# Performance work log

Hardware: AMD Instinct MI355X
Metric: run time of the kernel (lower is better)

Reference implementation:

```python
import jax, jax.numpy as jnp
from jax import lax
import numpy as np

U = 128  # num_units
F = 64   # input features
OUT = 6  # dense head units


def _lstm_layer(x, W, R, b):
    """Keras-style LSTM (gate order i,f,g,o; sigmoid recurrent act, tanh act).
    x: [B,T,D], W: [D,4U], R: [U,4U], b: [4U]. Returns (all_h [B,T,U], last_h [B,U])."""
    B = x.shape[0]
    xw = jnp.einsum('btd,dk->btk', x, W) + b  # precompute input projection [B,T,4U]

    def step(carry, xw_t):
        h, c = carry
        z = xw_t + h @ R  # [B,4U]
        i, f, g, o = jnp.split(z, 4, axis=-1)
        i = jax.nn.sigmoid(i)
        f = jax.nn.sigmoid(f)
        g = jnp.tanh(g)
        o = jax.nn.sigmoid(o)
        c = f * c + i * g
        h = o * jnp.tanh(c)
        return (h, c), h

    h0 = jnp.zeros((B, U), dtype=x.dtype)
    c0 = jnp.zeros((B, U), dtype=x.dtype)
    (h_last, _), hs = lax.scan(step, (h0, c0), jnp.swapaxes(xw, 0, 1))
    return jnp.swapaxes(hs, 0, 1), h_last


def setup_inputs() -> dict:
    key = jax.random.key(0)
    ks = jax.random.split(key, 12)
    s = 0.05
    inp = {
        'x': jax.random.normal(ks[0], (256, 512, F), dtype=jnp.float32),
        'W0': jax.random.normal(ks[1], (F, 4 * U), dtype=jnp.float32) * s,
        'R0': jax.random.normal(ks[2], (U, 4 * U), dtype=jnp.float32) * s,
        'b0': jnp.zeros((4 * U,), dtype=jnp.float32),
        'W1': jax.random.normal(ks[3], (U, 4 * U), dtype=jnp.float32) * s,
        'R1': jax.random.normal(ks[4], (U, 4 * U), dtype=jnp.float32) * s,
        'b1': jnp.zeros((4 * U,), dtype=jnp.float32),
        'W2': jax.random.normal(ks[5], (U, 4 * U), dtype=jnp.float32) * s,
        'R2': jax.random.normal(ks[6], (U, 4 * U), dtype=jnp.float32) * s,
        'b2': jnp.zeros((4 * U,), dtype=jnp.float32),
        'Wd': jax.random.normal(ks[7], (U, OUT), dtype=jnp.float32) * s,
        'bd': jnp.zeros((OUT,), dtype=jnp.float32),
    }
    return inp


def reference(x, W0, R0, b0, W1, R1, b1, W2, R2, b2, Wd, bd):
    h, _ = _lstm_layer(x, W0, R0, b0)      # [B,T,U]
    h, _ = _lstm_layer(h, W1, R1, b1)      # [B,T,U]
    _, h_last = _lstm_layer(h, W2, R2, b2) # [B,U] (return_sequences=False)
    return h_last @ Wd + bd                # [B,6]
```

## Files before the change

### kernel.cpp

```cpp
#include <hip/hip_runtime.h>
#include <cstdint>
#include <cstddef>

#define U4    512
#define UNITS 128
#define BATCH 256
#define TSEQ  512
#define FEAT  64
#define SEQS  8
#define NBLK  (BATCH / SEQS)

typedef short short8 __attribute__((ext_vector_type(8)));
typedef float f32x4  __attribute__((ext_vector_type(4)));

#define MFMA_BF16(C, A, B) \
    asm("v_mfma_f32_16x16x32_bf16 %0, %1, %2, %0" : "+v"(C) : "v"(A), "a"(B))

__device__ __forceinline__ void barrier_lds_only() {
    __builtin_amdgcn_sched_barrier(0);
    asm volatile("s_waitcnt lgkmcnt(0)" ::: "memory");
    __builtin_amdgcn_s_barrier();
    __builtin_amdgcn_sched_barrier(0);
}

__device__ __forceinline__ float sigm(float x) {
    float e = __expf(-x);
    return __fdividef(1.0f, 1.0f + e);
}
__device__ __forceinline__ float tanh_fast(float x) {
    float e = __expf(2.0f * x);
    return 1.0f - __fdividef(2.0f, e + 1.0f);
}

__device__ __forceinline__ unsigned short f2bf(float f) {
    unsigned u = __float_as_uint(f);
    unsigned r = u + 0x7FFFu + ((u >> 16) & 1u);
    return (unsigned short)(r >> 16);
}
__device__ __forceinline__ float bf2f(unsigned short h) {
    return __uint_as_float(((unsigned)h) << 16);
}

__global__ __launch_bounds__(256)
void rw_frag(const float* __restrict__ R0, const float* __restrict__ R1,
             const float* __restrict__ R2,
             const float* __restrict__ W0, const float* __restrict__ W1,
             const float* __restrict__ W2,
             unsigned short* __restrict__ Rf, unsigned short* __restrict__ Wf)
{
    if (blockIdx.x < 192) {
        int gid = blockIdx.x * 256 + threadIdx.x;
        int l    = gid >> 14;
        int r    = gid & 16383;
        int lane = r & 63;
        int fi   = r >> 6;
        int pass = fi & 1;
        int kt   = (fi >> 1) & 3;
        int gate = (fi >> 3) & 3;
        int w    = fi >> 5;
        const float* R = (l == 0) ? R0 : (l == 1) ? R1 : R2;

        int col = gate * UNITS + w * 16 + (lane & 15);
        int k0  = kt * 32 + (lane >> 4) * 8;
        short8 v;
        #pragma unroll
        for (int j = 0; j < 8; ++j) {
            float x = R[(size_t)(k0 + j) * U4 + col];
            unsigned short hi = f2bf(x);
            unsigned short s = pass ? f2bf(x - bf2f(hi)) : hi;
            v[j] = (short)s;
        }
        *(short8*)(Rf + (size_t)gid * 8) = v;
    } else {
        int gid = (blockIdx.x - 192) * 256 + threadIdx.x;
        int l    = gid >> 14;
        int r    = gid & 16383;
        int lane = r & 63;
        int fi   = r >> 6;
        int pass = fi & 1;
        int kt   = (fi >> 1) & 3;
        int nt   = fi >> 3;
        const float* W = (l == 0) ? W0 : (l == 1) ? W1 : W2;
        const int K = (l == 0) ? FEAT : UNITS;

        int col = nt * 16 + (lane & 15);
        int k0  = kt * 32 + (lane >> 4) * 8;
        short8 v;
        #pragma unroll
        for (int j = 0; j < 8; ++j) {
            float x = (k0 + j < K) ? W[(size_t)(k0 + j) * U4 + col] : 0.f;
            unsigned short hi = f2bf(x);
            unsigned short s = pass ? f2bf(x - bf2f(hi)) : hi;
            v[j] = (short)s;
        }
        *(short8*)(Wf + (size_t)gid * 8) = v;
    }
}

struct PCell {
    const float* in;
    float* out;
    const unsigned short* wf;
    const float* bias;
    int sB, sT, t0, K;
};
struct PStage { PCell c[3]; };

__global__ __launch_bounds__(512, 2)
void proj_mfma(PStage ps, int tcShift)
{
    const PCell ce = ps.c[blockIdx.y];
    const int tid  = threadIdx.x;
    const int lane = tid & 63;
    const int w    = tid >> 6;
    const int m    = lane & 15;
    const int quad = lane >> 4;
    const int TcMask = (1 << tcShift) - 1;
    const int m0 = blockIdx.x * 64;

    __shared__ __align__(16) unsigned short atab[8][16][136];

    short8 bf[4][4][2];
    #pragma unroll
    for (int nt = 0; nt < 4; ++nt)
        #pragma unroll
        for (int kt = 0; kt < 4; ++kt)
            #pragma unroll
            for (int pp = 0; pp < 2; ++pp)
                bf[nt][kt][pp] = *(const short8*)(
                    ce.wf + ((size_t)((((w * 4 + nt) * 4 + kt) * 2) + pp) * 64 + lane) * 8);

    const float* __restrict__ inp = ce.in;
    #pragma unroll
    for (int rep = 0; rep < 16; ++rep) {
        int idx = rep * 512 + tid;
        int row = idx >> 7;
        int k   = idx & 127;
        int rg  = m0 + row;
        int b = rg >> tcShift, tc = rg & TcMask;
        float x = 0.f;
        if (k < ce.K)
            x = inp[(size_t)b * ce.sB + (size_t)(ce.t0 + tc) * ce.sT + k];
        unsigned short hi = f2bf(x);
        atab[row >> 3][2 * (row & 7)][k]     = hi;
        atab[row >> 3][2 * (row & 7) + 1][k] = f2bf(x - bf2f(hi));
    }
    __syncthreads();

    float bb[4];
    #pragma unroll
    for (int nt = 0; nt < 4; ++nt) bb[nt] = ce.bias[w * 64 + nt * 16 + m];

    float* __restrict__ outp = ce.out;
    #pragma unroll 1
    for (int r = 0; r < 8; ++r) {
        short8 af[4];
        #pragma unroll
        for (int kt = 0; kt < 4; ++kt)
            af[kt] = *(const short8*)(&atab[r][m][kt * 32 + quad * 8]);

        f32x4 C[4];
        #pragma unroll
        for (int nt = 0; nt < 4; ++nt) C[nt] = f32x4{0.f, 0.f, 0.f, 0.f};

        #pragma unroll
        for (int kt = 0; kt < 4; ++kt)
            #pragma unroll
            for (int pp = 0; pp < 2; ++pp)
                #pragma unroll
                for (int nt = 0; nt < 4; ++nt)
                    MFMA_BF16(C[nt], af[kt], bf[nt][kt][pp]);

        int row0 = m0 + r * 8 + 2 * quad;
        #pragma unroll
        for (int nt = 0; nt < 4; ++nt) {
            float z0 = C[nt].x + C[nt].y + bb[nt];
            float z1 = C[nt].z + C[nt].w + bb[nt];
            int col = w * 64 + nt * 16 + m;
            outp[(size_t)row0 * U4 + col]       = z0;
            outp[(size_t)(row0 + 1) * U4 + col] = z1;
        }
    }
}

struct Cell {
    const float* xw;
    const unsigned short* rf;
    float* hs;
    float* cs;
    float* hout;
    int init;
    int pad_;
};
struct StageArgs { Cell c[3]; };

__global__ __launch_bounds__(512, 2)
void lstm_rec(StageArgs sa, int Tc)
{
    const Cell ce = sa.c[blockIdx.y];
    const float* __restrict__ xw = ce.xw;
    const unsigned short* __restrict__ Rf = ce.rf;
    float* __restrict__ h_state = ce.hs;
    float* __restrict__ c_state = ce.cs;
    float* __restrict__ h_out = ce.hout;
    const int init = ce.init;

    const int tid  = threadIdx.x;
    const int blk  = blockIdx.x;
    const int lane = tid & 63;
    const int w    = tid >> 6;
    const int m    = lane & 15;
    const int quad = lane >> 4;

    __shared__ __align__(16) unsigned short htab[2][16][136];

    short8 bf[4][4][2];
    #pragma unroll
    for (int g = 0; g < 4; ++g)
        #pragma unroll
        for (int kt = 0; kt < 4; ++kt)
            #pragma unroll
            for (int pp = 0; pp < 2; ++pp)
                bf[g][kt][pp] = *(const short8*)(
                    Rf + ((size_t)((((w * 4 + g) * 4 + kt) * 2) + pp) * 64 + lane) * 8);

    const int unit = w * 16 + m;
    const int s0   = 2 * quad;
    const int s1   = s0 + 1;

    float c0 = 0.f, c1 = 0.f;
    if (!init) {
        c0 = c_state[(blk * SEQS + s0) * UNITS + unit];
        c1 = c_state[(blk * SEQS + s1) * UNITS + unit];
    }
    {
        int uu = tid & 127;
        #pragma unroll
        for (int i = 0; i < 2; ++i) {
            int s = (tid >> 7) + i * 4;
            float hv = init ? 0.f : h_state[(blk * SEQS + s) * UNITS + uu];
            unsigned short hi = f2bf(hv);
            htab[0][2 * s][uu]     = hi;
            htab[0][2 * s + 1][uu] = f2bf(hv - bf2f(hi));
        }
    }
    __syncthreads();

    const float* xw0 = xw + (size_t)(blk * SEQS + s0) * Tc * U4 + unit;
    const float* xw1 = xw + (size_t)(blk * SEQS + s1) * Tc * U4 + unit;

    float xa[8], xb[8];
    #pragma unroll
    for (int g = 0; g < 4; ++g) {
        xa[g]     = xw0[g * UNITS];
        xa[4 + g] = xw1[g * UNITS];
    }
    {
        const size_t o1 = (size_t)((Tc > 1) ? 1 : 0) * U4;
        #pragma unroll
        for (int g = 0; g < 4; ++g) {
            xb[g]     = xw0[o1 + g * UNITS];
            xb[4 + g] = xw1[o1 + g * UNITS];
        }
    }

    float hl0 = 0.f, hl1 = 0.f;

    auto STEP = [&](int t, int p, float (&xc)[8]) {
        short8 af[4];
        #pragma unroll
        for (int kt = 0; kt < 4; ++kt)
            af[kt] = *(const short8*)(&htab[p][m][kt * 32 + quad * 8]);

        f32x4 C0 = {xc[0], 0.f, xc[4], 0.f};
        f32x4 C1 = {xc[1], 0.f, xc[5], 0.f};
        f32x4 C2 = {xc[2], 0.f, xc[6], 0.f};
        f32x4 C3 = {xc[3], 0.f, xc[7], 0.f};

        int tp = t + 2; if (tp >= Tc) tp = Tc - 1;
        const size_t off = (size_t)tp * U4;
        #pragma unroll
        for (int g = 0; g < 4; ++g) {
            xc[g]     = xw0[off + g * UNITS];
            xc[4 + g] = xw1[off + g * UNITS];
        }

        __builtin_amdgcn_s_setprio(1);
        #pragma unroll
        for (int kt = 0; kt < 4; ++kt) {
            #pragma unroll
            for (int pp = 0; pp < 2; ++pp) {
                MFMA_BF16(C0, af[kt], bf[0][kt][pp]);
                MFMA_BF16(C1, af[kt], bf[1][kt][pp]);
            }
        }

        float zi0 = C0.x + C0.y, zi1 = C0.z + C0.w;
        float zf0 = C1.x + C1.y, zf1 = C1.z + C1.w;
        float iv0 = sigm(zi0), iv1 = sigm(zi1);
        float fv0 = sigm(zf0), fv1 = sigm(zf1);

        #pragma unroll
        for (int kt = 0; kt < 4; ++kt) {
            #pragma unroll
            for (int pp = 0; pp < 2; ++pp) {
                MFMA_BF16(C2, af[kt], bf[2][kt][pp]);
                MFMA_BF16(C3, af[kt], bf[3][kt][pp]);
            }
        }
        __builtin_amdgcn_s_setprio(0);

        float zg0 = C2.x + C2.y, zg1 = C2.z + C2.w;
        float zo0 = C3.x + C3.y, zo1 = C3.z + C3.w;

        float gv0 = tanh_fast(zg0), ov0 = sigm(zo0);
        c0 = __builtin_fmaf(fv0, c0, iv0 * gv0);
        float hv0 = ov0 * tanh_fast(c0);

        float gv1 = tanh_fast(zg1), ov1 = sigm(zo1);
        c1 = __builtin_fmaf(fv1, c1, iv1 * gv1);
        float hv1 = ov1 * tanh_fast(c1);

        hl0 = hv0; hl1 = hv1;

        unsigned short hi0 = f2bf(hv0);
        htab[p ^ 1][4 * quad + 0][unit] = hi0;
        htab[p ^ 1][4 * quad + 1][unit] = f2bf(hv0 - bf2f(hi0));
        unsigned short hi1 = f2bf(hv1);
        htab[p ^ 1][4 * quad + 2][unit] = hi1;
        htab[p ^ 1][4 * quad + 3][unit] = f2bf(hv1 - bf2f(hi1));

        if (h_out) {
            h_out[((size_t)(blk * SEQS + s0) * Tc + t) * UNITS + unit] = hv0;
            h_out[((size_t)(blk * SEQS + s1) * Tc + t) * UNITS + unit] = hv1;
        }
        barrier_lds_only();
    };

    #pragma unroll 1
    for (int t = 0; t < Tc; t += 2) {
        STEP(t,     0, xa);
        STEP(t + 1, 1, xb);
    }

    c_state[(blk * SEQS + s0) * UNITS + unit] = c0;
    c_state[(blk * SEQS + s1) * UNITS + unit] = c1;
    h_state[(blk * SEQS + s0) * UNITS + unit] = hl0;
    h_state[(blk * SEQS + s1) * UNITS + unit] = hl1;
}

__global__ __launch_bounds__(256)
void dense_head(const float* __restrict__ h2, const float* __restrict__ Wd,
                const float* __restrict__ bd, float* __restrict__ out)
{
    int b = threadIdx.x;
    float acc[6];
    #pragma unroll
    for (int o = 0; o < 6; ++o) acc[o] = bd[o];
    #pragma unroll 4
    for (int k = 0; k < UNITS; ++k) {
        float hv = h2[b * UNITS + k];
        #pragma unroll
        for (int o = 0; o < 6; ++o)
            acc[o] = __builtin_fmaf(hv, Wd[k * 6 + o], acc[o]);
    }
    #pragma unroll
    for (int o = 0; o < 6; ++o) out[b * 6 + o] = acc[o];
}

extern "C" void kernel_launch(void* const* d_in, const int* in_sizes, int n_in,
                              void* d_out, int out_size, void* d_ws, size_t ws_size,
                              hipStream_t stream)
{
    (void)in_sizes; (void)n_in; (void)out_size;
    const float* x  = (const float*)d_in[0];
    const float* Ws[3] = {(const float*)d_in[1], (const float*)d_in[4], (const float*)d_in[7]};
    const float* Rs[3] = {(const float*)d_in[2], (const float*)d_in[5], (const float*)d_in[8]};
    const float* bs[3] = {(const float*)d_in[3], (const float*)d_in[6], (const float*)d_in[9]};
    const float* Wd = (const float*)d_in[10];
    const float* bd = (const float*)d_in[11];
    float* out = (float*)d_out;

    int tcShift = 6;
    while (tcShift > 2) {
        size_t need = ((size_t)1 << tcShift) * 1835008u + 2359296u;
        if (need <= ws_size) break;
        --tcShift;
    }
    const int Tc = 1 << tcShift;
    const int nCh = TSEQ / Tc;

    float* xw3 = (float*)d_ws;
    float* hc2 = xw3 + 3 * (size_t)BATCH * Tc * U4;
    float* hs  = hc2 + 2 * (size_t)BATCH * Tc * UNITS;
    float* cs  = hs + 3 * BATCH * UNITS;
    unsigned short* Rf = (unsigned short*)(cs + 3 * BATCH * UNITS);
    unsigned short* Wf = Rf + 3 * 131072;

    const size_t xwStride = (size_t)BATCH * Tc * U4;
    const size_t hcStride = (size_t)BATCH * Tc * UNITS;

    rw_frag<<<384, 256, 0, stream>>>(Rs[0], Rs[1], Rs[2], Ws[0], Ws[1], Ws[2], Rf, Wf);

    for (int s = 0; s <= nCh + 1; ++s) {
        int lo = s - (nCh - 1); if (lo < 0) lo = 0;
        int hi = (s < 2) ? s : 2;
        if (lo > hi) continue;

        PStage ps{};
        StageArgs sa{};
        int n = 0;
        for (int lam = lo; lam <= hi; ++lam) {
            int c = s - lam;
            ps.c[n].in   = (lam == 0) ? x : hc2 + (size_t)(lam - 1) * hcStride;
            ps.c[n].out  = xw3 + (size_t)lam * xwStride;
            ps.c[n].wf   = Wf + (size_t)lam * 131072;
            ps.c[n].bias = bs[lam];
            ps.c[n].sB   = (lam == 0) ? TSEQ * FEAT : Tc * UNITS;
            ps.c[n].sT   = (lam == 0) ? FEAT : UNITS;
            ps.c[n].t0   = (lam == 0) ? c * Tc : 0;
            ps.c[n].K    = (lam == 0) ? FEAT : UNITS;

            sa.c[n].xw   = xw3 + (size_t)lam * xwStride;
            sa.c[n].rf   = Rf + (size_t)lam * 131072;
            sa.c[n].hs   = hs + lam * BATCH * UNITS;
            sa.c[n].cs   = cs + lam * BATCH * UNITS;
            sa.c[n].hout = (lam < 2) ? (hc2 + (size_t)lam * hcStride) : nullptr;
            sa.c[n].init = (c == 0) ? 1 : 0;
            ++n;
        }
        proj_mfma<<<dim3(BATCH * Tc / 64, n), 512, 0, stream>>>(ps, tcShift);
        lstm_rec<<<dim3(NBLK, n), 512, 0, stream>>>(sa, Tc);
    }

    dense_head<<<1, 256, 0, stream>>>(hs + 2 * BATCH * UNITS, Wd, bd, out);
}
```

Before: 1.266 ms.

## Fuse next-chunk layer-0 projection into recurrent stage kernel and pack hidden-state splits

Layer-0 input projection for the next chunk now runs as extra blocks inside the same launch as the recurrent LSTM blocks. Its output goes to a double-buffered xw slot, so the projection work can fill CUs the 32-96 recurrent blocks leave idle. Hidden-state outputs for the next layer are stored as packed bf16 hi/lo pairs, so the following projection skips the float-to-bf16 split and reads 4-byte words. The cost is more workspace, a larger shared-memory footprint for recurrent blocks, and a separate projection launch for layers 1-2.

```diff
diff --git a/kernel.cpp b/kernel.cpp
--- a/kernel.cpp
+++ b/kernel.cpp
@@ -12,6 +12,7 @@
 
 typedef short short8 __attribute__((ext_vector_type(8)));
 typedef float f32x4  __attribute__((ext_vector_type(4)));
+typedef unsigned short tab_t[16][136];
 
 #define MFMA_BF16(C, A, B) \
     asm("v_mfma_f32_16x16x32_bf16 %0, %1, %2, %0" : "+v"(C) : "v"(A), "a"(B))
@@ -98,27 +99,24 @@
 }
 
 struct PCell {
-    const float* in;
+    const void* in;
     float* out;
     const unsigned short* wf;
     const float* bias;
-    int sB, sT, t0, K;
+    int sB, sT, t0, K, packed, pad_;
 };
-struct PStage { PCell c[3]; };
-
-__global__ __launch_bounds__(512, 2)
-void proj_mfma(PStage ps, int tcShift)
-{
-    const PCell ce = ps.c[blockIdx.y];
+struct PStage { PCell c[2]; };
+
+__device__ __forceinline__ void proj_body(const PCell& ce, int bx, int tcShift,
+                                          tab_t* __restrict__ atab)
+{
     const int tid  = threadIdx.x;
     const int lane = tid & 63;
     const int w    = tid >> 6;
     const int m    = lane & 15;
     const int quad = lane >> 4;
     const int TcMask = (1 << tcShift) - 1;
-    const int m0 = blockIdx.x * 64;
-
-    __shared__ __align__(16) unsigned short atab[8][16][136];
+    const int m0 = bx * 64;
 
     short8 bf[4][4][2];
     #pragma unroll
@@ -130,20 +128,35 @@
                 bf[nt][kt][pp] = *(const short8*)(
                     ce.wf + ((size_t)((((w * 4 + nt) * 4 + kt) * 2) + pp) * 64 + lane) * 8);
 
-    const float* __restrict__ inp = ce.in;
-    #pragma unroll
-    for (int rep = 0; rep < 16; ++rep) {
-        int idx = rep * 512 + tid;
-        int row = idx >> 7;
-        int k   = idx & 127;
-        int rg  = m0 + row;
-        int b = rg >> tcShift, tc = rg & TcMask;
-        float x = 0.f;
-        if (k < ce.K)
-            x = inp[(size_t)b * ce.sB + (size_t)(ce.t0 + tc) * ce.sT + k];
-        unsigned short hi = f2bf(x);
-        atab[row >> 3][2 * (row & 7)][k]     = hi;
-        atab[row >> 3][2 * (row & 7) + 1][k] = f2bf(x - bf2f(hi));
+    if (ce.packed) {
+        const unsigned int* __restrict__ inp = (const unsigned int*)ce.in;
+        #pragma unroll
+        for (int rep = 0; rep < 16; ++rep) {
+            int idx = rep * 512 + tid;
+            int row = idx >> 7;
+            int k   = idx & 127;
+            int rg  = m0 + row;
+            int b = rg >> tcShift, tc = rg & TcMask;
+            unsigned int u = inp[(size_t)b * ce.sB + (size_t)(ce.t0 + tc) * ce.sT + k];
+            atab[row >> 3][2 * (row & 7)][k]     = (unsigned short)(u & 0xFFFFu);
+            atab[row >> 3][2 * (row & 7) + 1][k] = (unsigned short)(u >> 16);
+        }
+    } else {
+        const float* __restrict__ inp = (const float*)ce.in;
+        #pragma unroll
+        for (int rep = 0; rep < 16; ++rep) {
+            int idx = rep * 512 + tid;
+            int row = idx >> 7;
+            int k   = idx & 127;
+            int rg  = m0 + row;
+            int b = rg >> tcShift, tc = rg & TcMask;
+            float x = 0.f;
+            if (k < ce.K)
+                x = inp[(size_t)b * ce.sB + (size_t)(ce.t0 + tc) * ce.sT + k];
+            unsigned short hi = f2bf(x);
+            atab[row >> 3][2 * (row & 7)][k]     = hi;
+            atab[row >> 3][2 * (row & 7) + 1][k] = f2bf(x - bf2f(hi));
+        }
     }
     __syncthreads();
 
@@ -183,36 +196,38 @@
     }
 }
 
+__global__ __launch_bounds__(512, 2)
+void proj_mfma(PStage ps, int tcShift)
+{
+    __shared__ __align__(16) unsigned short smem[8 * 16 * 136];
+    proj_body(ps.c[blockIdx.y], blockIdx.x, tcShift, (tab_t*)smem);
+}
+
 struct Cell {
     const float* xw;
     const unsigned short* rf;
     float* hs;
     float* cs;
-    float* hout;
+    unsigned int* hout;
     int init;
     int pad_;
 };
-struct StageArgs { Cell c[3]; };
-
-__global__ __launch_bounds__(512, 2)
-void lstm_rec(StageArgs sa, int Tc)
-{
-    const Cell ce = sa.c[blockIdx.y];
+
+__device__ __forceinline__ void lstm_body(const Cell& ce, int blk, int Tc,
+                                          tab_t* __restrict__ htab)
+{
     const float* __restrict__ xw = ce.xw;
     const unsigned short* __restrict__ Rf = ce.rf;
     float* __restrict__ h_state = ce.hs;
     float* __restrict__ c_state = ce.cs;
-    float* __restrict__ h_out = ce.hout;
+    unsigned int* __restrict__ h_out = ce.hout;
     const int init = ce.init;
 
     const int tid  = threadIdx.x;
-    const int blk  = blockIdx.x;
     const int lane = tid & 63;
     const int w    = tid >> 6;
     const int m    = lane & 15;
     const int quad = lane >> 4;
-
-    __shared__ __align__(16) unsigned short htab[2][16][136];
 
     short8 bf[4][4][2];
     #pragma unroll
@@ -294,7 +309,6 @@
                 MFMA_BF16(C1, af[kt], bf[1][kt][pp]);
             }
         }
-
         float zi0 = C0.x + C0.y, zi1 = C0.z + C0.w;
         float zf0 = C1.x + C1.y, zf1 = C1.z + C1.w;
         float iv0 = sigm(zi0), iv1 = sigm(zi1);
@@ -324,15 +338,19 @@
         hl0 = hv0; hl1 = hv1;
 
         unsigned short hi0 = f2bf(hv0);
+        unsigned short lo0 = f2bf(hv0 - bf2f(hi0));
         htab[p ^ 1][4 * quad + 0][unit] = hi0;
-        htab[p ^ 1][4 * quad + 1][unit] = f2bf(hv0 - bf2f(hi0));
+        htab[p ^ 1][4 * quad + 1][unit] = lo0;
         unsigned short hi1 = f2bf(hv1);
+        unsigned short lo1 = f2bf(hv1 - bf2f(hi1));
         htab[p ^ 1][4 * quad + 2][unit] = hi1;
-        htab[p ^ 1][4 * quad + 3][unit] = f2bf(hv1 - bf2f(hi1));
+        htab[p ^ 1][4 * quad + 3][unit] = lo1;
 
         if (h_out) {
-            h_out[((size_t)(blk * SEQS + s0) * Tc + t) * UNITS + unit] = hv0;
-            h_out[((size_t)(blk * SEQS + s1) * Tc + t) * UNITS + unit] = hv1;
+            h_out[((size_t)(blk * SEQS + s0) * Tc + t) * UNITS + unit] =
+                (unsigned int)hi0 | ((unsigned int)lo0 << 16);
+            h_out[((size_t)(blk * SEQS + s1) * Tc + t) * UNITS + unit] =
+                (unsigned int)hi1 | ((unsigned int)lo1 << 16);
         }
         barrier_lds_only();
     };
@@ -347,6 +365,24 @@
     c_state[(blk * SEQS + s1) * UNITS + unit] = c1;
     h_state[(blk * SEQS + s0) * UNITS + unit] = hl0;
     h_state[(blk * SEQS + s1) * UNITS + unit] = hl1;
+}
+
+struct FusedArgs {
+    Cell lc[3];
+    PCell pc;
+    int n_lstm;
+    int has_proj;
+};
+
+__global__ __launch_bounds__(512, 2)
+void stage_fused(FusedArgs fa, int Tc, int tcShift)
+{
+    __shared__ __align__(16) unsigned short smem[8 * 16 * 136];
+    int bx = blockIdx.x;
+    if (bx < fa.n_lstm * NBLK)
+        lstm_body(fa.lc[bx >> 5], bx & 31, Tc, (tab_t*)smem);
+    else
+        proj_body(fa.pc, bx - fa.n_lstm * NBLK, tcShift, (tab_t*)smem);
 }
 
 __global__ __launch_bounds__(256)
@@ -383,24 +419,33 @@
 
     int tcShift = 6;
     while (tcShift > 2) {
-        size_t need = ((size_t)1 << tcShift) * 1835008u + 2359296u;
+        size_t need = ((size_t)1 << tcShift) * 2359296u + 2359296u;
         if (need <= ws_size) break;
         --tcShift;
     }
     const int Tc = 1 << tcShift;
     const int nCh = TSEQ / Tc;
-
-    float* xw3 = (float*)d_ws;
-    float* hc2 = xw3 + 3 * (size_t)BATCH * Tc * U4;
-    float* hs  = hc2 + 2 * (size_t)BATCH * Tc * UNITS;
-    float* cs  = hs + 3 * BATCH * UNITS;
+    const int projGrid = BATCH * Tc / 64;
+
+    const size_t xwStride = (size_t)BATCH * Tc * U4;
+    const size_t hcStride = (size_t)BATCH * Tc * UNITS;
+
+    float* xw = (float*)d_ws;
+    unsigned int* hc = (unsigned int*)(xw + 4 * xwStride);
+    float* hs = (float*)(hc + 2 * hcStride);
+    float* cs = hs + 3 * BATCH * UNITS;
     unsigned short* Rf = (unsigned short*)(cs + 3 * BATCH * UNITS);
     unsigned short* Wf = Rf + 3 * 131072;
 
-    const size_t xwStride = (size_t)BATCH * Tc * U4;
-    const size_t hcStride = (size_t)BATCH * Tc * UNITS;
-
     rw_frag<<<384, 256, 0, stream>>>(Rs[0], Rs[1], Rs[2], Ws[0], Ws[1], Ws[2], Rf, Wf);
+
+    {
+        PStage ps{};
+        ps.c[0].in = x; ps.c[0].out = xw; ps.c[0].wf = Wf; ps.c[0].bias = bs[0];
+        ps.c[0].sB = TSEQ * FEAT; ps.c[0].sT = FEAT; ps.c[0].t0 = 0;
+        ps.c[0].K = FEAT; ps.c[0].packed = 0;
+        proj_mfma<<<dim3(projGrid, 1), 512, 0, stream>>>(ps, tcShift);
+    }
 
     for (int s = 0; s <= nCh + 1; ++s) {
         int lo = s - (nCh - 1); if (lo < 0) lo = 0;
@@ -408,29 +453,46 @@
         if (lo > hi) continue;
 
         PStage ps{};
-        StageArgs sa{};
+        int pn = 0;
+        int plo = (lo > 1) ? lo : 1;
+        for (int lam = plo; lam <= hi; ++lam) {
+            ps.c[pn].in   = hc + (size_t)(lam - 1) * hcStride;
+            ps.c[pn].out  = xw + (size_t)(1 + lam) * xwStride;
+            ps.c[pn].wf   = Wf + (size_t)lam * 131072;
+            ps.c[pn].bias = bs[lam];
+            ps.c[pn].sB   = Tc * UNITS;
+            ps.c[pn].sT   = UNITS;
+            ps.c[pn].t0   = 0;
+            ps.c[pn].K    = UNITS;
+            ps.c[pn].packed = 1;
+            ++pn;
+        }
+        if (pn) proj_mfma<<<dim3(projGrid, pn), 512, 0, stream>>>(ps, tcShift);
+
+        FusedArgs fa{};
         int n = 0;
         for (int lam = lo; lam <= hi; ++lam) {
             int c = s - lam;
-            ps.c[n].in   = (lam == 0) ? x : hc2 + (size_t)(lam - 1) * hcStride;
-            ps.c[n].out  = xw3 + (size_t)lam * xwStride;
-            ps.c[n].wf   = Wf + (size_t)lam * 131072;
-            ps.c[n].bias = bs[lam];
-            ps.c[n].sB   = (lam == 0) ? TSEQ * FEAT : Tc * UNITS;
-            ps.c[n].sT   = (lam == 0) ? FEAT : UNITS;
-            ps.c[n].t0   = (lam == 0) ? c * Tc : 0;
-            ps.c[n].K    = (lam == 0) ? FEAT : UNITS;
-
-            sa.c[n].xw   = xw3 + (size_t)lam * xwStride;
-            sa.c[n].rf   = Rf + (size_t)lam * 131072;
-            sa.c[n].hs   = hs + lam * BATCH * UNITS;
-            sa.c[n].cs   = cs + lam * BATCH * UNITS;
-            sa.c[n].hout = (lam < 2) ? (hc2 + (size_t)lam * hcStride) : nullptr;
-            sa.c[n].init = (c == 0) ? 1 : 0;
+            fa.lc[n].xw   = (lam == 0) ? xw + (size_t)(c & 1) * xwStride
+                                       : xw + (size_t)(1 + lam) * xwStride;
+            fa.lc[n].rf   = Rf + (size_t)lam * 131072;
+            fa.lc[n].hs   = hs + lam * BATCH * UNITS;
+            fa.lc[n].cs   = cs + lam * BATCH * UNITS;
+            fa.lc[n].hout = (lam < 2) ? (hc + (size_t)lam * hcStride) : nullptr;
+            fa.lc[n].init = (c == 0) ? 1 : 0;
             ++n;
         }
-        proj_mfma<<<dim3(BATCH * Tc / 64, n), 512, 0, stream>>>(ps, tcShift);
-        lstm_rec<<<dim3(NBLK, n), 512, 0, stream>>>(sa, Tc);
+        fa.n_lstm = n;
+        int c0 = s + 1;
+        fa.has_proj = (c0 <= nCh - 1) ? 1 : 0;
+        if (fa.has_proj) {
+            fa.pc.in = x; fa.pc.out = xw + (size_t)(c0 & 1) * xwStride;
+            fa.pc.wf = Wf; fa.pc.bias = bs[0];
+            fa.pc.sB = TSEQ * FEAT; fa.pc.sT = FEAT; fa.pc.t0 = c0 * Tc;
+            fa.pc.K = FEAT; fa.pc.packed = 0;
+        }
+        int gridx = n * NBLK + (fa.has_proj ? projGrid : 0);
+        stage_fused<<<dim3(gridx), 512, 0, stream>>>(fa, Tc, tcShift);
     }
 
     dense_head<<<1, 256, 0, stream>>>(hs + 2 * BATCH * UNITS, Wd, bd, out);
```

Result: faster. 1.119 ms, median of 2 (-11.6%).
